# Kernel tuning notes

Hardware: AMD Instinct MI355X
Metric: run time of the kernel (lower is better)

Reference implementation:

```python
import jax, jax.numpy as jnp
import numpy as np

K_TOP = 4
NUM_EXPERTS = 8


def _lstm_dir(x, wih, whh, b):
    # x: [B,T,in], wih: [4H,in], whh: [4H,H], b: [4H] (b_ih+b_hh)
    xW = jnp.einsum('bti,gi->btg', x, wih) + b  # [B,T,4H]
    B = x.shape[0]
    H = whh.shape[1]
    init = (jnp.zeros((B, H), x.dtype), jnp.zeros((B, H), x.dtype))

    def step(carry, xt):
        h, c = carry
        g = xt + h @ whh.T
        i, f, gg, o = jnp.split(g, 4, axis=-1)  # torch gate order i,f,g,o
        c = jax.nn.sigmoid(f) * c + jax.nn.sigmoid(i) * jnp.tanh(gg)
        h = jax.nn.sigmoid(o) * jnp.tanh(c)
        return (h, c), h

    _, hs = jax.lax.scan(step, init, jnp.swapaxes(xW, 0, 1))  # [T,B,H]
    return jnp.swapaxes(hs, 0, 1)


def _bidir_layer(x, Wih, Whh, bih, bhh):
    # Wih: [2,4H,in]; dir 0 forward, dir 1 backward
    hf = _lstm_dir(x, Wih[0], Whh[0], bih[0] + bhh[0])
    hb = _lstm_dir(x[:, ::-1], Wih[1], Whh[1], bih[1] + bhh[1])[:, ::-1]
    return jnp.concatenate([hf, hb], axis=-1)  # [B,T,2H]


def _expert(x, Wih0, Whh0, bih0, bhh0, Wih1, Whh1, bih1, bhh1):
    h = _bidir_layer(x, Wih0, Whh0, bih0, bhh0)   # [B,T,2H]
    h = _bidir_layer(h, Wih1, Whh1, bih1, bhh1)   # [B,T,2H]
    return h


def _cv_squared(v):
    v = v.astype(jnp.float32)
    return jnp.var(v, ddof=1) / (jnp.mean(v) ** 2 + 1e-10)


def _forward(x, spk, wg_w, wg_b, Wih0, Whh0, bih0, bhh0, Wih1, Whh1, bih1, bhh1, fc1_w, fc1_b, fc_w, fc_b, loss_coef=0.01):
    B, T, _ = x.shape
    # --- top-k gating (eval path: clean logits, no noise) ---
    logits = spk @ wg_w.T + wg_b                      # [B,E]
    top_vals, top_idx = jax.lax.top_k(logits, K_TOP + 1)
    gates_k = jax.nn.softmax(top_vals[:, :K_TOP], axis=-1)
    rows = jnp.arange(B)[:, None]
    gates = jnp.zeros_like(logits).at[rows, top_idx[:, :K_TOP]].set(gates_k)  # [B,E]
    load = (gates > 0).sum(0)
    importance = gates.sum(0)
    loss = (_cv_squared(importance) + _cv_squared(load)) * loss_coef
    # --- run all experts (dense mixture, as in source) ---
    expert_h = jax.vmap(_expert, in_axes=(None, 0, 0, 0, 0, 0, 0, 0, 0))(
        x, Wih0, Whh0, bih0, bhh0, Wih1, Whh1, bih1, bhh1)          # [E,B,T,2H]
    expert_out = jnp.einsum('ebtf,hf->ebth', expert_h, fc1_w) + fc1_b  # [E,B,T,H]
    data_output = jnp.einsum('ebth,be->bth', expert_out, gates)        # [B,T,H]
    out = jnp.einsum('bth,oh->bto', data_output, fc_w) + fc_b          # [B,T,O]
    out = jnp.swapaxes(out, 0, 1)                                      # [T,B,O]
    return out, loss


def setup_inputs() -> dict:
    key = jax.random.key(0)
    ks = jax.random.split(key, 16)
    B, T, D, H, E, O, S = 32, 1024, 128, 128, 8, 44, 256
    s = 0.08  # weight scale to keep LSTM gates in sane range
    return {
        'x': jax.random.normal(ks[0], (B, T, D), jnp.float32),
        'spk': jax.random.normal(ks[1], (B, S), jnp.float32),
        'wg_w': jax.random.normal(ks[2], (E, S), jnp.float32) * s,
        'wg_b': jax.random.normal(ks[3], (E,), jnp.float32) * s,
        'Wih0': jax.random.normal(ks[4], (E, 2, 4 * H, D), jnp.float32) * s,
        'Whh0': jax.random.normal(ks[5], (E, 2, 4 * H, H), jnp.float32) * s,
        'bih0': jax.random.normal(ks[6], (E, 2, 4 * H), jnp.float32) * s,
        'bhh0': jax.random.normal(ks[7], (E, 2, 4 * H), jnp.float32) * s,
        'Wih1': jax.random.normal(ks[8], (E, 2, 4 * H, 2 * H), jnp.float32) * s,
        'Whh1': jax.random.normal(ks[9], (E, 2, 4 * H, H), jnp.float32) * s,
        'bih1': jax.random.normal(ks[10], (E, 2, 4 * H), jnp.float32) * s,
        'bhh1': jax.random.normal(ks[11], (E, 2, 4 * H), jnp.float32) * s,
        'fc1_w': jax.random.normal(ks[12], (H, 2 * H), jnp.float32) * s,
        'fc1_b': jax.random.normal(ks[13], (H,), jnp.float32) * s,
        'fc_w': jax.random.normal(ks[14], (O, H), jnp.float32) * s,
        'fc_b': jax.random.normal(ks[15], (O,), jnp.float32) * s,
    }


def reference(x, spk, wg_w, wg_b, Wih0, Whh0, bih0, bhh0, Wih1, Whh1, bih1, bhh1, fc1_w, fc1_b, fc_w, fc_b):
    return _forward(x, spk, wg_w, wg_b, Wih0, Whh0, bih0, bhh0, Wih1, Whh1, bih1, bhh1, fc1_w, fc1_b, fc_w, fc_b)
```

## Files before the change

### kernel.cpp

```cpp
#include <hip/hip_runtime.h>

typedef __attribute__((ext_vector_type(4))) float f32x4;
typedef __attribute__((ext_vector_type(8))) short s16x8;

#define LOG2E 1.4426950408889634f
#define K2L   2.8853900817779268f

__device__ __forceinline__ unsigned short f2bf(float f) {
  union { float f; unsigned int i; } v; v.f = f;
  unsigned int u = v.i;
  u = (u + 0x7FFFu + ((u >> 16) & 1u)) >> 16;
  return (unsigned short)u;
}
__device__ __forceinline__ float bf2f(unsigned short s) {
  union { unsigned int i; float f; } v; v.i = ((unsigned int)s) << 16;
  return v.f;
}
__device__ __forceinline__ float rcp_(float x) { return __builtin_amdgcn_rcpf(x); }
__device__ __forceinline__ float ex2(float x) { return __builtin_amdgcn_exp2f(x); }
__device__ __forceinline__ f32x4 mfma16(s16x8 a, s16x8 b, f32x4 c) {
  return __builtin_amdgcn_mfma_f32_16x16x32_bf16(a, b, c, 0, 0, 0);
}
__device__ __forceinline__ s16x8 pack8s(const float* s, float sc) {
  s16x8 v;
#pragma unroll
  for (int j = 0; j < 8; ++j) v[j] = (short)f2bf(s[j] * sc);
  return v;
}

#define OFF_H0   0
#define OFF_XW   134217728
#define OFF_XT   201326592
#define OFF_WHH  209715200
#define OFF_H1C  213909504
#define OFF_HST  230686720
#define OFF_CST  230817792
#define OFF_M    231079936
#define OFF_CV   231129088
#define OFF_G    231129344
#define WS_NEED  231130368

__global__ void wsdbg_kernel(float* __restrict__ out, float v) { out[0] = v; }

__global__ void prepw_kernel(const float* __restrict__ Whh0, const float* __restrict__ Whh1,
                             unsigned short* __restrict__ whhb) {
  const int i = blockIdx.x * 512 + threadIdx.x;
  if (i < 2097152) {
    const int gate = (i >> 14) & 3;
    const float sc = (gate == 2) ? K2L : -LOG2E;
    whhb[i] = f2bf((i < 1048576 ? Whh0[i] : Whh1[i - 1048576]) * sc);
  }
}

__global__ void prepx_kernel(const float* __restrict__ x, unsigned short* __restrict__ xt) {
  const int i = blockIdx.x * 512 + threadIdx.x;
  for (int j = i; j < 4194304; j += 2097152) {
    const int b = j >> 17, rem = j & 131071, t = rem >> 7, f = rem & 127;
    xt[((size_t)t * 32 + b) * 128 + f] = f2bf(x[j]);
  }
}

__global__ void mprep_kernel(const float* __restrict__ fc1w, const float* __restrict__ fc1b,
                             const float* __restrict__ fcw, const float* __restrict__ fcb,
                             float* __restrict__ M, float* __restrict__ Cv) {
  const int mi = blockIdx.x * 256 + threadIdx.x;
  if (mi < 12288) {
    const int dd = mi / 6144, rem = mi % 6144, o = rem >> 7, hc = rem & 127;
    float s = 0.f;
    if (o < 44)
      for (int h = 0; h < 128; ++h) s += fcw[o * 128 + h] * fc1w[h * 256 + dd * 128 + hc];
    M[mi] = s;
  }
  if (blockIdx.x == 0 && threadIdx.x < 44) {
    const int o = threadIdx.x;
    float s = fcb[o];
    for (int h = 0; h < 128; ++h) s += fcw[o * 128 + h] * fc1b[h];
    Cv[o] = s;
  }
}

__global__ void initout_kernel(const float* __restrict__ Cv, float* __restrict__ out) {
  const int i = blockIdx.x * 512 + threadIdx.x;
  if (i < 1441792) out[i] = Cv[i % 44];
}

__global__ void gating_kernel(const float* __restrict__ spk,
                              const float* __restrict__ wgw,
                              const float* __restrict__ wgb,
                              float* __restrict__ gates_out,
                              float* __restrict__ loss_out) {
  __shared__ __align__(16) float logits[32][8];
  __shared__ __align__(16) float gmat[32][8];
  const int tid = threadIdx.x;
  {
    const int b = tid >> 3, e = tid & 7;
    float s = wgb[e];
    for (int k = 0; k < 256; ++k) s += spk[b * 256 + k] * wgw[e * 256 + k];
    logits[b][e] = s;
  }
  __syncthreads();
  if (tid < 32) {
    const int b = tid;
    float v[8];
    for (int e = 0; e < 8; ++e) v[e] = logits[b][e];
    int idx[4]; float val[4];
    unsigned used = 0;
    for (int k = 0; k < 4; ++k) {
      float best = -1e30f; int bi = 0;
      for (int e = 0; e < 8; ++e)
        if (!((used >> e) & 1) && v[e] > best) { best = v[e]; bi = e; }
      used |= (1u << bi); idx[k] = bi; val[k] = best;
    }
    const float m = val[0];
    float ex[4], ssum = 0.f;
    for (int k = 0; k < 4; ++k) { ex[k] = ex2(LOG2E * (val[k] - m)); ssum += ex[k]; }
    for (int e = 0; e < 8; ++e) gmat[b][e] = 0.f;
    for (int k = 0; k < 4; ++k) gmat[b][idx[k]] = ex[k] / ssum;
    for (int e = 0; e < 8; ++e) gates_out[b * 8 + e] = gmat[b][e];
  }
  __syncthreads();
  if (tid == 0) {
    float imp[8], ld[8];
    for (int e = 0; e < 8; ++e) {
      float si = 0.f, sl = 0.f;
      for (int b = 0; b < 32; ++b) { si += gmat[b][e]; sl += (gmat[b][e] > 0.f) ? 1.f : 0.f; }
      imp[e] = si; ld[e] = sl;
    }
    float mi = 0.f, ml = 0.f;
    for (int e = 0; e < 8; ++e) { mi += imp[e]; ml += ld[e]; }
    mi *= 0.125f; ml *= 0.125f;
    float vi = 0.f, vl = 0.f;
    for (int e = 0; e < 8; ++e) {
      vi += (imp[e] - mi) * (imp[e] - mi);
      vl += (ld[e] - ml) * (ld[e] - ml);
    }
    vi /= 7.f; vl /= 7.f;
    loss_out[0] = 0.01f * (vi / (mi * mi + 1e-10f) + vl / (ml * ml + 1e-10f));
  }
}

template <int L>
__global__ __launch_bounds__(512, 1) void fused(
    int k,
    const unsigned short* __restrict__ Asrc,
    const float* __restrict__ Wih, const float* __restrict__ bihp, const float* __restrict__ bhhp,
    const unsigned short* __restrict__ whhb,
    unsigned short* __restrict__ xwbufs,
    unsigned short* __restrict__ hstate, float* __restrict__ cstate,
    unsigned short* __restrict__ hout,
    const float* __restrict__ Mmat, const float* __restrict__ gatesp,
    float* __restrict__ outp) {
  constexpr int KC = L ? 8 : 4;
  constexpr int KS = KC * 32;
  const int tid = threadIdx.x, w = tid >> 6, l = tid & 63;
  const int l15 = l & 15, lq = l >> 4;

  if (L && blockIdx.x >= 192) {
    const int c2 = k - 2;
    if (c2 < 0 || c2 > 15) return;
    if (w >= 6) return;
    const int ss = blockIdx.x - 192;
    const int mt = (w >= 3) ? 1 : 0, ot = w - mt * 3;
    const int o = ot * 16 + l15;
    const bool ov = o < 44;
    s16x8 bfm[2][4];
#pragma unroll
    for (int dd = 0; dd < 2; ++dd)
#pragma unroll
      for (int kc = 0; kc < 4; ++kc) {
        if (ov) bfm[dd][kc] = pack8s(Mmat + ((size_t)dd * 48 + o) * 128 + kc * 32 + lq * 8, 1.f);
        else { s16x8 z = {0,0,0,0,0,0,0,0}; bfm[dd][kc] = z; }
      }
    const unsigned short* hb = hout + (size_t)(c2 & 1) * 4194304;
    f32x4 acc0 = {0.f,0.f,0.f,0.f}, acc1 = {0.f,0.f,0.f,0.f};
    for (int e = 0; e < 8; ++e) {
      const unsigned short* ap = hb + ((((size_t)e * 64 + ss) * 32) + mt * 16 + l15) * 256 + lq * 8;
      f32x4 p0 = {0.f,0.f,0.f,0.f}, p1 = {0.f,0.f,0.f,0.f};
#pragma unroll
      for (int kc = 0; kc < 4; ++kc) {
        s16x8 a0 = *(const s16x8*)(ap + kc * 32);
        s16x8 a1 = *(const s16x8*)(ap + 128 + kc * 32);
        p0 = mfma16(a0, bfm[0][kc], p0);
        p1 = mfma16(a1, bfm[1][kc], p1);
      }
#pragma unroll
      for (int r = 0; r < 4; ++r) {
        const float g = gatesp[(mt * 16 + lq * 4 + r) * 8 + e];
        acc0[r] += g * p0[r];
        acc1[r] += g * p1[r];
      }
    }
    if (ov) {
      const int s2 = c2 * 64 + ss, t1 = 1023 - s2;
#pragma unroll
      for (int r = 0; r < 4; ++r) {
        const int b = mt * 16 + lq * 4 + r;
        outp[((size_t)s2 * 32 + b) * 44 + o] += acc0[r];
        outp[((size_t)t1 * 32 + b) * 44 + o] += acc1[r];
      }
    }
    return;
  }

  if (blockIdx.x >= 32) {
    if (k >= 16) return;
    const int gb = blockIdx.x - 32;
    const int ed = gb & 15, e = ed >> 1, d = ed & 1;
    const int slice = gb >> 4;
    const int nsl = L ? 10 : 14;
    unsigned short* xw = xwbufs + (size_t)(k & 1) * 16777216;

    s16x8 bf[4][KC];
    float bias[4];
#pragma unroll
    for (int j = 0; j < 4; ++j) {
      const int n = w * 64 + j * 16 + l15;
      const float sc = ((n >> 7) == 2) ? K2L : -LOG2E;
      bias[j] = (bihp[ed * 512 + n] + bhhp[ed * 512 + n]) * sc;
      const float* wp = Wih + ((size_t)ed * 512 + n) * KS + lq * 8;
#pragma unroll
      for (int kc = 0; kc < KC; ++kc) bf[j][kc] = pack8s(wp + kc * 32, sc);
    }
    for (int ss = slice; ss < 64; ss += nsl) {
      const int s = k * 64 + ss;
      const int t = d ? 1023 - s : s;
#pragma unroll
      for (int mt = 0; mt < 2; ++mt) {
        const size_t arow = (size_t)(L ? (e * 1024 + t) : t) * 32 + mt * 16 + l15;
        const unsigned short* ap = Asrc + arow * KS + lq * 8;
        s16x8 af[KC];
#pragma unroll
        for (int kc = 0; kc < KC; ++kc) af[kc] = *(const s16x8*)(ap + kc * 32);
        f32x4 acc[4];
#pragma unroll
        for (int j = 0; j < 4; ++j) acc[j] = f32x4{bias[j], bias[j], bias[j], bias[j]};
#pragma unroll
        for (int kc = 0; kc < KC; ++kc) {
#pragma unroll
          for (int j = 0; j < 4; ++j) acc[j] = mfma16(af[kc], bf[j][kc], acc[j]);
        }
        unsigned short* op = xw + (((size_t)(ed * 2 + mt) * 64 + ss) * 512) * 16 + lq * 4;
#pragma unroll
        for (int j = 0; j < 4; ++j) {
          const int n = w * 64 + j * 16 + l15;
          ushort4 o4;
          o4.x = f2bf(acc[j][0]); o4.y = f2bf(acc[j][1]);
          o4.z = f2bf(acc[j][2]); o4.w = f2bf(acc[j][3]);
          *(ushort4*)(op + (size_t)n * 16) = o4;
        }
      }
    }
    return;
  }

  const int c = k - 1;
  if (c < 0 || c > 15) return;
  const int rb = blockIdx.x, ed2 = rb >> 1, bh = rb & 1;
  const int e = ed2 >> 1, d = ed2 & 1;
  __shared__ __align__(16) char hbf[2][4096];
  const int cell = w * 16 + l15;

  s16x8 bfh[4][4];
#pragma unroll
  for (int g = 0; g < 4; ++g) {
    const unsigned short* wp = whhb + ((size_t)ed2 * 512 + g * 128 + cell) * 128 + lq * 8;
#pragma unroll
    for (int kc = 0; kc < 4; ++kc) bfh[g][kc] = *(const s16x8*)(wp + kc * 32);
  }
  const int wb0 = ((cell >> 5) << 10) | (((cell >> 3) & 3) << 8) | ((cell & 7) << 1);
  float cst[4];
  unsigned short hb4[4];
  if (c == 0) {
#pragma unroll
    for (int r = 0; r < 4; ++r) { cst[r] = 0.f; hb4[r] = 0; }
    if (tid < 256) {
      s16x8 z = {0,0,0,0,0,0,0,0};
      *(s16x8*)(&hbf[0][tid * 16]) = z;
    }
  } else {
    const float* cp = cstate + ((size_t)rb * 512 + tid) * 4;
    const unsigned short* hp = hstate + ((size_t)rb * 512 + tid) * 4;
#pragma unroll
    for (int r = 0; r < 4; ++r) {
      cst[r] = cp[r];
      hb4[r] = hp[r];
      *(unsigned short*)(&hbf[0][wb0 | ((lq * 4 + r) << 4)]) = hp[r];
    }
  }
  __syncthreads();

  const unsigned short* xwb =
      xwbufs + (size_t)(c & 1) * 16777216 + ((size_t)(ed2 * 2 + bh) * 64) * 8192 + cell * 16 + lq * 4;
  const int brow = bh * 16 + lq * 4;

  ushort4 xq[4];
#pragma unroll
  for (int g = 0; g < 4; ++g) xq[g] = *(const ushort4*)(xwb + g * 2048);

  for (int tt = 0; tt < 64; ++tt) {
    const int p = tt & 1;
    ushort4 nxq[4];
    {
      const int tn = tt < 63 ? tt + 1 : 63;
#pragma unroll
      for (int g = 0; g < 4; ++g) nxq[g] = *(const ushort4*)(xwb + (size_t)tn * 8192 + g * 2048);
    }
    if (tt > 0) {
      const int ptt = tt - 1;
      size_t ob;
      if (L) {
        ob = (size_t)(c & 1) * 4194304 + (((size_t)e * 64 + ptt) * 32 + brow) * 256 + d * 128 + cell;
      } else {
        const int s = c * 64 + ptt;
        const int tg = d ? 1023 - s : s;
        ob = (((size_t)e * 1024 + tg) * 32 + brow) * 256 + d * 128 + cell;
      }
#pragma unroll
      for (int r = 0; r < 4; ++r) hout[ob + (size_t)r * 256] = hb4[r];
    }

    s16x8 hf[4];
#pragma unroll
    for (int kc = 0; kc < 4; ++kc) hf[kc] = *(const s16x8*)(&hbf[p][kc * 1024 + l * 16]);
    f32x4 a[4];
#pragma unroll
    for (int g = 0; g < 4; ++g) {
      a[g][0] = bf2f(xq[g].x); a[g][1] = bf2f(xq[g].y);
      a[g][2] = bf2f(xq[g].z); a[g][3] = bf2f(xq[g].w);
    }
#pragma unroll
    for (int kc = 0; kc < 4; ++kc) {
#pragma unroll
      for (int g = 0; g < 4; ++g) a[g] = mfma16(hf[kc], bfh[g][kc], a[g]);
    }

#pragma unroll
    for (int r = 0; r < 4; ++r) {
      const float ai = ex2(a[0][r]);
      const float af = ex2(a[1][r]);
      const float bg = ex2(fminf(a[2][r], 80.f));
      const float ao = ex2(a[3][r]);
      const float sf = rcp_(1.f + af);
      const float r1 = rcp_((1.f + ai) * (1.f + bg));
      const float bgm = __builtin_fmaf(bg, K2L, -K2L);
      const float cc = __builtin_fmaf(sf, cst[r], bgm * r1);
      cst[r] = cc;
      const float qc = ex2(fminf(cc, 80.f));
      const float r2 = rcp_((1.f + ao) * (1.f + qc));
      hb4[r] = f2bf((qc - 1.f) * r2);
    }
    char* hw = &hbf[1 - p][0];
#pragma unroll
    for (int r = 0; r < 4; ++r)
      *(unsigned short*)(hw + (wb0 | ((lq * 4 + r) << 4))) = hb4[r];
    __syncthreads();
#pragma unroll
    for (int g = 0; g < 4; ++g) xq[g] = nxq[g];
  }

  {
    size_t ob;
    if (L) {
      ob = (size_t)(c & 1) * 4194304 + (((size_t)e * 64 + 63) * 32 + brow) * 256 + d * 128 + cell;
    } else {
      const int s = c * 64 + 63;
      const int tg = d ? 1023 - s : s;
      ob = (((size_t)e * 1024 + tg) * 32 + brow) * 256 + d * 128 + cell;
    }
#pragma unroll
    for (int r = 0; r < 4; ++r) hout[ob + (size_t)r * 256] = hb4[r];
    unsigned short* hsp = hstate + ((size_t)rb * 512 + tid) * 4;
    float* csp = cstate + ((size_t)rb * 512 + tid) * 4;
#pragma unroll
    for (int r = 0; r < 4; ++r) { hsp[r] = hb4[r]; csp[r] = cst[r]; }
  }
}

extern "C" void kernel_launch(void* const* d_in, const int* in_sizes, int n_in,
                              void* d_out, int out_size, void* d_ws, size_t ws_size,
                              hipStream_t stream) {
  const float* x    = (const float*)d_in[0];
  const float* spk  = (const float*)d_in[1];
  const float* wgw  = (const float*)d_in[2];
  const float* wgb  = (const float*)d_in[3];
  const float* Wih0 = (const float*)d_in[4];
  const float* Whh0 = (const float*)d_in[5];
  const float* bih0 = (const float*)d_in[6];
  const float* bhh0 = (const float*)d_in[7];
  const float* Wih1 = (const float*)d_in[8];
  const float* Whh1 = (const float*)d_in[9];
  const float* bih1 = (const float*)d_in[10];
  const float* bhh1 = (const float*)d_in[11];
  const float* fc1w = (const float*)d_in[12];
  const float* fc1b = (const float*)d_in[13];
  const float* fcw  = (const float*)d_in[14];
  const float* fcb  = (const float*)d_in[15];
  float* out = (float*)d_out;

  if (ws_size < (size_t)WS_NEED) {
    wsdbg_kernel<<<1, 1, 0, stream>>>(out, (float)(ws_size >> 20));
    return;
  }
  char* ws = (char*)d_ws;
  unsigned short* h0     = (unsigned short*)(ws + OFF_H0);
  unsigned short* xwbufs = (unsigned short*)(ws + OFF_XW);
  unsigned short* xt     = (unsigned short*)(ws + OFF_XT);
  unsigned short* whhb   = (unsigned short*)(ws + OFF_WHH);
  unsigned short* h1c    = (unsigned short*)(ws + OFF_H1C);
  unsigned short* hstate = (unsigned short*)(ws + OFF_HST);
  float*          cstate = (float*)(ws + OFF_CST);
  float*          Mmat   = (float*)(ws + OFF_M);
  float*          Cv     = (float*)(ws + OFF_CV);
  float*          gatesw = (float*)(ws + OFF_G);

  prepw_kernel<<<4096, 512, 0, stream>>>(Whh0, Whh1, whhb);
  prepx_kernel<<<4096, 512, 0, stream>>>(x, xt);
  mprep_kernel<<<48, 256, 0, stream>>>(fc1w, fc1b, fcw, fcb, Mmat, Cv);
  initout_kernel<<<2816, 512, 0, stream>>>(Cv, out);
  gating_kernel<<<1, 256, 0, stream>>>(spk, wgw, wgb, gatesw, out + 1441792);

  for (int k = 0; k <= 16; ++k)
    fused<0><<<256, 512, 0, stream>>>(k, xt, Wih0, bih0, bhh0, whhb, xwbufs,
                                      hstate, cstate, h0, nullptr, nullptr, out);
  for (int k = 0; k <= 17; ++k)
    fused<1><<<256, 512, 0, stream>>>(k, h0, Wih1, bih1, bhh1, whhb + 1048576, xwbufs,
                                      hstate, cstate, h1c, Mmat, gatesw, out);
}
```

Measured before the change: 2.076 ms.

## Pre-convert Wih to bf16, prefetch xW two steps ahead, streamline LSTM cell math

```diff
diff --git a/kernel.cpp b/kernel.cpp
--- a/kernel.cpp
+++ b/kernel.cpp
@@ -27,6 +27,8 @@
   for (int j = 0; j < 8; ++j) v[j] = (short)f2bf(s[j] * sc);
   return v;
 }
+
+#define BARRIER_LGKM() asm volatile("s_waitcnt lgkmcnt(0)\n\ts_barrier" ::: "memory")
 
 #define OFF_H0   0
 #define OFF_XW   134217728
@@ -38,17 +40,45 @@
 #define OFF_M    231079936
 #define OFF_CV   231129088
 #define OFF_G    231129344
-#define WS_NEED  231130368
+#define OFF_WIH0 231130368
+#define OFF_WIH1 233227520
+#define OFF_BIA  237421824
+#define WS_NEED  237552896
 
 __global__ void wsdbg_kernel(float* __restrict__ out, float v) { out[0] = v; }
 
-__global__ void prepw_kernel(const float* __restrict__ Whh0, const float* __restrict__ Whh1,
-                             unsigned short* __restrict__ whhb) {
-  const int i = blockIdx.x * 512 + threadIdx.x;
-  if (i < 2097152) {
-    const int gate = (i >> 14) & 3;
+__global__ void prep_kernel(const float* __restrict__ Whh0, const float* __restrict__ Whh1,
+                            const float* __restrict__ Wih0, const float* __restrict__ Wih1,
+                            const float* __restrict__ bih0, const float* __restrict__ bhh0,
+                            const float* __restrict__ bih1, const float* __restrict__ bhh1,
+                            unsigned short* __restrict__ whhb,
+                            unsigned short* __restrict__ wihb0,
+                            unsigned short* __restrict__ wihb1,
+                            float* __restrict__ biasb) {
+  const int tid = blockIdx.x * 512 + threadIdx.x;
+  for (int i = tid; i < 5242880; i += 2097152) {
+    if (i < 2097152) {
+      const int gate = (i >> 14) & 3;
+      const float sc = (gate == 2) ? K2L : -LOG2E;
+      whhb[i] = f2bf((i < 1048576 ? Whh0[i] : Whh1[i - 1048576]) * sc);
+    } else if (i < 3145728) {
+      const int j = i - 2097152;
+      const int gate = (j >> 14) & 3;
+      const float sc = (gate == 2) ? K2L : -LOG2E;
+      wihb0[j] = f2bf(Wih0[j] * sc);
+    } else {
+      const int j = i - 3145728;
+      const int gate = (j >> 15) & 3;
+      const float sc = (gate == 2) ? K2L : -LOG2E;
+      wihb1[j] = f2bf(Wih1[j] * sc);
+    }
+  }
+  if (tid < 16384) {
+    const int L = tid >> 13, rem = tid & 8191;
+    const int gate = (rem >> 7) & 3;
     const float sc = (gate == 2) ? K2L : -LOG2E;
-    whhb[i] = f2bf((i < 1048576 ? Whh0[i] : Whh1[i - 1048576]) * sc);
+    const float b = L ? (bih1[rem] + bhh1[rem]) : (bih0[rem] + bhh0[rem]);
+    biasb[tid] = b * sc;
   }
 }
 
@@ -143,7 +173,8 @@
 __global__ __launch_bounds__(512, 1) void fused(
     int k,
     const unsigned short* __restrict__ Asrc,
-    const float* __restrict__ Wih, const float* __restrict__ bihp, const float* __restrict__ bhhp,
+    const unsigned short* __restrict__ wihb,
+    const float* __restrict__ biasb,
     const unsigned short* __restrict__ whhb,
     unsigned short* __restrict__ xwbufs,
     unsigned short* __restrict__ hstate, float* __restrict__ cstate,
@@ -215,11 +246,10 @@
 #pragma unroll
     for (int j = 0; j < 4; ++j) {
       const int n = w * 64 + j * 16 + l15;
-      const float sc = ((n >> 7) == 2) ? K2L : -LOG2E;
-      bias[j] = (bihp[ed * 512 + n] + bhhp[ed * 512 + n]) * sc;
-      const float* wp = Wih + ((size_t)ed * 512 + n) * KS + lq * 8;
-#pragma unroll
-      for (int kc = 0; kc < KC; ++kc) bf[j][kc] = pack8s(wp + kc * 32, sc);
+      bias[j] = biasb[ed * 512 + n];
+      const unsigned short* wp = wihb + ((size_t)ed * 512 + n) * KS + lq * 8;
+#pragma unroll
+      for (int kc = 0; kc < KC; ++kc) bf[j][kc] = *(const s16x8*)(wp + kc * 32);
     }
     for (int ss = slice; ss < 64; ss += nsl) {
       const int s = k * 64 + ss;
@@ -293,17 +323,25 @@
       xwbufs + (size_t)(c & 1) * 16777216 + ((size_t)(ed2 * 2 + bh) * 64) * 8192 + cell * 16 + lq * 4;
   const int brow = bh * 16 + lq * 4;
 
-  ushort4 xq[4];
-#pragma unroll
-  for (int g = 0; g < 4; ++g) xq[g] = *(const ushort4*)(xwb + g * 2048);
-
-  for (int tt = 0; tt < 64; ++tt) {
+  ushort4 xqA[4], xqB[4];
+#pragma unroll
+  for (int g = 0; g < 4; ++g) {
+    xqA[g] = *(const ushort4*)(xwb + g * 2048);
+    xqB[g] = *(const ushort4*)(xwb + 8192 + g * 2048);
+  }
+
+  auto step = [&](int tt, ushort4* xq) {
     const int p = tt & 1;
-    ushort4 nxq[4];
+    f32x4 a[4];
+#pragma unroll
+    for (int g = 0; g < 4; ++g) {
+      a[g][0] = bf2f(xq[g].x); a[g][1] = bf2f(xq[g].y);
+      a[g][2] = bf2f(xq[g].z); a[g][3] = bf2f(xq[g].w);
+    }
     {
-      const int tn = tt < 63 ? tt + 1 : 63;
-#pragma unroll
-      for (int g = 0; g < 4; ++g) nxq[g] = *(const ushort4*)(xwb + (size_t)tn * 8192 + g * 2048);
+      const int tn = tt < 62 ? tt + 2 : 63;
+#pragma unroll
+      for (int g = 0; g < 4; ++g) xq[g] = *(const ushort4*)(xwb + (size_t)tn * 8192 + g * 2048);
     }
     if (tt > 0) {
       const int ptt = tt - 1;
@@ -318,32 +356,26 @@
 #pragma unroll
       for (int r = 0; r < 4; ++r) hout[ob + (size_t)r * 256] = hb4[r];
     }
-
     s16x8 hf[4];
 #pragma unroll
     for (int kc = 0; kc < 4; ++kc) hf[kc] = *(const s16x8*)(&hbf[p][kc * 1024 + l * 16]);
-    f32x4 a[4];
-#pragma unroll
-    for (int g = 0; g < 4; ++g) {
-      a[g][0] = bf2f(xq[g].x); a[g][1] = bf2f(xq[g].y);
-      a[g][2] = bf2f(xq[g].z); a[g][3] = bf2f(xq[g].w);
-    }
 #pragma unroll
     for (int kc = 0; kc < 4; ++kc) {
 #pragma unroll
       for (int g = 0; g < 4; ++g) a[g] = mfma16(hf[kc], bfh[g][kc], a[g]);
     }
-
 #pragma unroll
     for (int r = 0; r < 4; ++r) {
-      const float ai = ex2(a[0][r]);
-      const float af = ex2(a[1][r]);
+      const float ai = ex2(fminf(a[0][r], 23.f));
+      const float af = ex2(fminf(a[1][r], 23.f));
       const float bg = ex2(fminf(a[2][r], 80.f));
-      const float ao = ex2(a[3][r]);
-      const float sf = rcp_(1.f + af);
-      const float r1 = rcp_((1.f + ai) * (1.f + bg));
+      const float ao = ex2(fminf(a[3][r], 23.f));
+      const float pai = 1.f + ai, paf = 1.f + af, pbg = 1.f + bg;
+      const float t1 = pai * pbg;
+      const float r1 = rcp_(paf * t1);
       const float bgm = __builtin_fmaf(bg, K2L, -K2L);
-      const float cc = __builtin_fmaf(sf, cst[r], bgm * r1);
+      const float num = __builtin_fmaf(bgm, paf, cst[r] * t1);
+      const float cc = num * r1;
       cst[r] = cc;
       const float qc = ex2(fminf(cc, 80.f));
       const float r2 = rcp_((1.f + ao) * (1.f + qc));
@@ -353,9 +385,12 @@
 #pragma unroll
     for (int r = 0; r < 4; ++r)
       *(unsigned short*)(hw + (wb0 | ((lq * 4 + r) << 4))) = hb4[r];
-    __syncthreads();
-#pragma unroll
-    for (int g = 0; g < 4; ++g) xq[g] = nxq[g];
+    BARRIER_LGKM();
+  };
+
+  for (int t2 = 0; t2 < 64; t2 += 2) {
+    step(t2, xqA);
+    step(t2 + 1, xqB);
   }
 
   {
@@ -412,17 +447,21 @@
   float*          Mmat   = (float*)(ws + OFF_M);
   float*          Cv     = (float*)(ws + OFF_CV);
   float*          gatesw = (float*)(ws + OFF_G);
-
-  prepw_kernel<<<4096, 512, 0, stream>>>(Whh0, Whh1, whhb);
+  unsigned short* wihb0  = (unsigned short*)(ws + OFF_WIH0);
+  unsigned short* wihb1  = (unsigned short*)(ws + OFF_WIH1);
+  float*          biasb  = (float*)(ws + OFF_BIA);
+
+  prep_kernel<<<4096, 512, 0, stream>>>(Whh0, Whh1, Wih0, Wih1, bih0, bhh0, bih1, bhh1,
+                                        whhb, wihb0, wihb1, biasb);
   prepx_kernel<<<4096, 512, 0, stream>>>(x, xt);
   mprep_kernel<<<48, 256, 0, stream>>>(fc1w, fc1b, fcw, fcb, Mmat, Cv);
   initout_kernel<<<2816, 512, 0, stream>>>(Cv, out);
   gating_kernel<<<1, 256, 0, stream>>>(spk, wgw, wgb, gatesw, out + 1441792);
 
   for (int k = 0; k <= 16; ++k)
-    fused<0><<<256, 512, 0, stream>>>(k, xt, Wih0, bih0, bhh0, whhb, xwbufs,
+    fused<0><<<256, 512, 0, stream>>>(k, xt, wihb0, biasb, whhb, xwbufs,
                                       hstate, cstate, h0, nullptr, nullptr, out);
   for (int k = 0; k <= 17; ++k)
-    fused<1><<<256, 512, 0, stream>>>(k, h0, Wih1, bih1, bhh1, whhb + 1048576, xwbufs,
+    fused<1><<<256, 512, 0, stream>>>(k, h0, wihb1, biasb + 8192, whhb + 1048576, xwbufs,
                                       hstate, cstate, h1c, Mmat, gatesw, out);
 }
```

New measurement: 2.491 ms. 20.0% more time.
